# Optimization experiments

Measured on AMD Instinct MI355X. Metric: run time of the kernel, lower is better.

The kernel has to match this reference:

```python
import jax, jax.numpy as jnp
import numpy as np

B, S, D, E = 8, 2048, 1024, 8
TOKENS = B * S
CAPACITY = TOKENS // E  # capacity_factor=1.0, top-1 gating (deepspeed default)


def _moe_layer(x_flat, Wg, We, be):
    """DeepSpeed-style top-1 MoE: gate -> capacity drop -> dispatch -> expert GEMM -> combine.
    x_flat: [T, D]; Wg: [D, E]; We: [E, D, D]; be: [E, D]."""
    gates = jax.nn.softmax(x_flat @ Wg, axis=-1)              # [T, E]
    idx = jnp.argmax(gates, axis=1)                            # [T] expert per token
    mask = jax.nn.one_hot(idx, E, dtype=jnp.int32)             # [T, E]
    loc = jnp.cumsum(mask, axis=0) - 1                         # position within expert
    loc_s = jnp.sum(loc * mask, axis=1)                        # [T]
    keep = loc_s < CAPACITY                                    # capacity drop
    gate_s = jnp.sum(gates * mask.astype(gates.dtype), axis=1) * keep.astype(gates.dtype)
    slot = jnp.clip(loc_s, 0, CAPACITY - 1)
    # dispatch: scatter kept tokens into [E, C, D] buffer (slots are unique for kept tokens)
    disp = jnp.zeros((E, CAPACITY, D), x_flat.dtype).at[idx, slot].add(
        x_flat * keep[:, None].astype(x_flat.dtype))
    # grouped expert GEMM
    eo = jnp.einsum('ecd,edf->ecf', disp, We) + be[:, None, :]  # [E, C, D]
    # combine: gather each token's expert output, scale by its gate value
    return eo[idx, slot] * gate_s[:, None]                      # [T, D]


def reference(x, y, W1, b1, Wg2, We2, be2, Wg3, We3, be3):
    h = jnp.einsum('bsd,df->bsf', x, W1) + b1                  # dense pre-layer
    hf = h.reshape(TOKENS, D)
    o = _moe_layer(hf, Wg2, We2, be2)
    o = _moe_layer(o, Wg3, We3, be3)
    h = h + o.reshape(B, S, D)                                 # residual add
    sent = h.mean(axis=1)                                      # [B, D]
    logp = jax.nn.log_softmax(sent, axis=-1)
    return -jnp.mean(logp[jnp.arange(B), y])                   # CrossEntropyLoss


def setup_inputs() -> dict:
    key = jax.random.key(0)
    ks = jax.random.split(key, 10)
    s = 0.02
    return {
        'x': jax.random.normal(ks[0], (B, S, D), jnp.float32),
        'y': jax.random.randint(ks[1], (B,), 0, D),
        'W1': jax.random.normal(ks[2], (D, D), jnp.float32) * s,
        'b1': jnp.zeros((D,), jnp.float32),
        'Wg2': jax.random.normal(ks[3], (D, E), jnp.float32) * s,
        'We2': jax.random.normal(ks[4], (E, D, D), jnp.float32) * s,
        'be2': jnp.zeros((E, D), jnp.float32),
        'Wg3': jax.random.normal(ks[5], (D, E), jnp.float32) * s,
        'We3': jax.random.normal(ks[6], (E, D, D), jnp.float32) * s,
        'be3': jnp.zeros((E, D), jnp.float32),
    }
```

## Files before the change

kernel.cpp:

```cpp
#include <hip/hip_runtime.h>
#include <hip/hip_bf16.h>
#include <math.h>


#define TOKS 16384
#define DIM 1024
#define NEXP 8
#define CAP 2048
#define BATCH 8
#define SEQ 2048

typedef __bf16 bf16_t;
typedef __bf16 bf16x8 __attribute__((ext_vector_type(8)));
typedef float fx4 __attribute__((ext_vector_type(4)));

__device__ __forceinline__ void gll16(const bf16_t* g, bf16_t* l) {
  __builtin_amdgcn_global_load_lds(
      (const __attribute__((address_space(1))) unsigned int*)g,
      (__attribute__((address_space(3))) unsigned int*)l, 16, 0, 0);
}

#define PW_BLOCKS (17 * 256)
#define CVT_BLOCKS (TOKS * DIM / 8 / 256)
#define PREP_GRID (PW_BLOCKS + 2 + CVT_BLOCKS + 1)
__global__ __launch_bounds__(256) void k_prep(
    const float* __restrict__ W1, const float* __restrict__ We2,
    const float* __restrict__ We3, const float* __restrict__ Wg2,
    const float* __restrict__ Wg3, const float* __restrict__ x,
    bf16_t* __restrict__ Wt, bf16_t* __restrict__ WgP,
    bf16_t* __restrict__ xb, uint4* __restrict__ zreg, int znq) {
  const int id = blockIdx.x;
  const int tid = threadIdx.x;
  if (id < PW_BLOCKS) {
    __shared__ float t[64][65];
    const int m = id >> 8, rem = id & 255;
    const int n0 = (rem & 15) * 64, k0 = (rem >> 4) * 64;
    const float* src = (m == 0) ? W1
                       : (m <= 8) ? We2 + (size_t)(m - 1) * DIM * DIM
                                  : We3 + (size_t)(m - 9) * DIM * DIM;
    bf16_t* dst = Wt + (size_t)m * DIM * DIM;
    const int r = tid >> 4, c4 = (tid & 15) * 4;
#pragma unroll
    for (int i = 0; i < 4; i++) {
      float4 v = *(const float4*)&src[(size_t)(k0 + i * 16 + r) * DIM + n0 + c4];
      t[i * 16 + r][c4] = v.x;
      t[i * 16 + r][c4 + 1] = v.y;
      t[i * 16 + r][c4 + 2] = v.z;
      t[i * 16 + r][c4 + 3] = v.w;
    }
    __syncthreads();
#pragma unroll
    for (int i = 0; i < 4; i++) {
      int rn = i * 16 + r;
      union { bf16_t b[4]; uint2 u; } tmp;
#pragma unroll
      for (int j = 0; j < 4; j++) tmp.b[j] = (bf16_t)t[c4 + j][rn];
      *(uint2*)&dst[(size_t)(n0 + rn) * DIM + k0 + c4] = tmp.u;
    }
  } else if (id < PW_BLOCKS + 2) {
    const int which = id - PW_BLOCKS;
    const float* src = which ? Wg3 : Wg2;
    bf16_t* dst = WgP + which * (128 * 8 * 8);
#pragma unroll
    for (int j = 0; j < 4; j++) {
      int d = tid * 4 + j;
      float4 a = *(const float4*)&src[d * 8];
      float4 b = *(const float4*)&src[d * 8 + 4];
      float v[8] = {a.x, a.y, a.z, a.w, b.x, b.y, b.z, b.w};
#pragma unroll
      for (int e = 0; e < 8; e++)
        dst[((d >> 3) * 8 + e) * 8 + (d & 7)] = (bf16_t)v[e];
    }
  } else if (id < PW_BLOCKS + 2 + CVT_BLOCKS) {
    const int cid = id - PW_BLOCKS - 2;
    size_t i = ((size_t)cid * 256 + tid) * 8;
    float4 a = *(const float4*)&x[i];
    float4 b = *(const float4*)&x[i + 4];
    union { bf16_t h[8]; uint4 u; } t;
    t.h[0] = (bf16_t)a.x; t.h[1] = (bf16_t)a.y; t.h[2] = (bf16_t)a.z; t.h[3] = (bf16_t)a.w;
    t.h[4] = (bf16_t)b.x; t.h[5] = (bf16_t)b.y; t.h[6] = (bf16_t)b.z; t.h[7] = (bf16_t)b.w;
    *(uint4*)&xb[i] = t.u;
  } else {
    const uint4 z = {0u, 0u, 0u, 0u};
    for (int i = tid; i < znq; i += 256) zreg[i] = z;
  }
}

__global__ __launch_bounds__(256) void k_gemm_dense(
    const bf16_t* __restrict__ A, const bf16_t* __restrict__ Bt,
    const float* __restrict__ bias, bf16_t* __restrict__ out,
    float* __restrict__ sent) {
  __shared__ alignas(16) bf16_t As[128 * 64];
  __shared__ alignas(16) bf16_t Bs[128 * 64];
  const int tid = threadIdx.x;
  const int lane = tid & 63, wave = tid >> 6;
  const int quad = lane >> 4, l15 = lane & 15;
  const int wr = (wave >> 1) * 64, wc = (wave & 1) * 64;
  const int id = blockIdx.x;
  const int j_ = id >> 3;
  const int m0 = ((id & 7) * 16 + (j_ >> 3)) * 128;
  const int n0 = (j_ & 7) * 128;
  const int kc = (tid & 7) ^ ((tid >> 3) & 7);
  const int rbase = tid >> 3;

  const bf16_t* gA[4]; const bf16_t* gB[4]; bf16_t* lA[4]; bf16_t* lB[4];
#pragma unroll
  for (int i = 0; i < 4; i++) {
    int r = rbase + 32 * i;
    gA[i] = A + (size_t)(m0 + r) * DIM + kc * 8;
    gB[i] = Bt + (size_t)(n0 + r) * DIM + kc * 8;
    lA[i] = &As[(wave * 64 + 256 * i) * 8];
    lB[i] = &Bs[(wave * 64 + 256 * i) * 8];
  }
  fx4 acc[4][4];
#pragma unroll
  for (int i = 0; i < 4; i++)
#pragma unroll
    for (int j = 0; j < 4; j++) acc[i][j] = (fx4)0.0f;

  for (int k0 = 0; k0 < DIM; k0 += 64) {
#pragma unroll
    for (int i = 0; i < 4; i++) gll16(gA[i] + k0, lA[i]);
#pragma unroll
    for (int i = 0; i < 4; i++) gll16(gB[i] + k0, lB[i]);
    __syncthreads();
#pragma unroll
    for (int s = 0; s < 2; s++) {
      const int pofs = ((s * 4 + quad) ^ (l15 & 7)) << 3;
      bf16x8 av[4], bv[4];
#pragma unroll
      for (int i = 0; i < 4; i++)
        av[i] = *(const bf16x8*)&As[(wr + i * 16 + l15) * 64 + pofs];
#pragma unroll
      for (int j = 0; j < 4; j++)
        bv[j] = *(const bf16x8*)&Bs[(wc + j * 16 + l15) * 64 + pofs];
#pragma unroll
      for (int i = 0; i < 4; i++)
#pragma unroll
        for (int j = 0; j < 4; j++)
          acc[i][j] = __builtin_amdgcn_mfma_f32_16x16x32_bf16(av[i], bv[j], acc[i][j], 0, 0, 0);
    }
    __syncthreads();
  }
  float bb[4], sj[4] = {0.f, 0.f, 0.f, 0.f};
#pragma unroll
  for (int j = 0; j < 4; j++) bb[j] = bias[n0 + wc + j * 16 + l15];
#pragma unroll
  for (int i = 0; i < 4; i++)
#pragma unroll
    for (int r = 0; r < 4; r++) {
      int rowL = wr + i * 16 + quad * 4 + r;
#pragma unroll
      for (int j = 0; j < 4; j++) {
        float v = acc[i][j][r] + bb[j];
        sj[j] += v;
        out[(size_t)(m0 + rowL) * DIM + n0 + wc + j * 16 + l15] = (bf16_t)v;
      }
    }
#pragma unroll
  for (int j = 0; j < 4; j++) {
    sj[j] += __shfl_xor(sj[j], 16);
    sj[j] += __shfl_xor(sj[j], 32);
  }
  if (quad == 0) {
#pragma unroll
    for (int j = 0; j < 4; j++)
      atomicAdd(&sent[(m0 >> 11) * DIM + n0 + wc + j * 16 + l15],
                sj[j] * (1.0f / SEQ));
  }
}

__global__ __launch_bounds__(256) void k_gate_mm(
    const bf16_t* __restrict__ act, const bf16_t* __restrict__ WgPx,
    int* __restrict__ idx, float* __restrict__ gate) {
  __shared__ alignas(16) bf16_t As[64 * 64];
  __shared__ alignas(16) bf16_t WgS[128 * 64];
  __shared__ float L[64][8];
  const int tid = threadIdx.x;
  const int lane = tid & 63, wave = tid >> 6;
  const int quad = lane >> 4, l15 = lane & 15;
  const int m0 = blockIdx.x * 64;
  const int kc = (tid & 7) ^ ((tid >> 3) & 7);
  const int rbase = tid >> 3;

#pragma unroll
  for (int j = 0; j < 4; j++)
    gll16(WgPx + (j * 256 + wave * 64 + lane) * 8, &WgS[(j * 256 + wave * 64) * 8]);

  const bf16_t* gA[2]; bf16_t* lA[2];
#pragma unroll
  for (int i = 0; i < 2; i++) {
    gA[i] = act + (size_t)(m0 + rbase + 32 * i) * DIM + kc * 8;
    lA[i] = &As[wave * 512 + i * 2048];
  }
  fx4 acc = (fx4)0.0f;
  for (int k0 = 0; k0 < DIM; k0 += 64) {
#pragma unroll
    for (int i = 0; i < 2; i++) gll16(gA[i] + k0, lA[i]);
    __syncthreads();
#pragma unroll
    for (int s = 0; s < 2; s++) {
      const int pofs = ((s * 4 + quad) ^ (l15 & 7)) << 3;
      bf16x8 av = *(const bf16x8*)&As[(wave * 16 + l15) * 64 + pofs];
      bf16x8 bv = *(const bf16x8*)&WgS[((k0 >> 3) + s * 4 + quad) * 64 + (l15 & 7) * 8];
      acc = __builtin_amdgcn_mfma_f32_16x16x32_bf16(av, bv, acc, 0, 0, 0);
    }
    __syncthreads();
  }
  if (l15 < 8) {
#pragma unroll
    for (int r = 0; r < 4; r++) L[wave * 16 + quad * 4 + r][l15] = acc[r];
  }
  __syncthreads();
  if (tid < 64) {
    float lg[8];
#pragma unroll
    for (int e = 0; e < 8; e++) lg[e] = L[tid][e];
    float best = lg[0];
    int bi = 0;
#pragma unroll
    for (int e = 1; e < 8; e++)
      if (lg[e] > best) { best = lg[e]; bi = e; }
    float s = 0.f;
#pragma unroll
    for (int e = 0; e < 8; e++) s += expf(lg[e] - best);
    idx[m0 + tid] = bi;
    gate[m0 + tid] = 1.0f / s;
  }
}

#define DLMAX 2048
__global__ __launch_bounds__(1024) void k_route(
    const int* __restrict__ idx, int* __restrict__ tok, int* __restrict__ cnt,
    bf16_t* __restrict__ obuf) {
  const int e = blockIdx.x;
  const int tid = threadIdx.x, lane = tid & 63, wv = tid >> 6;
  __shared__ int wsum[16];
  __shared__ int dlist[DLMAX];
  const int4* p = (const int4*)(idx + tid * 16);
  int m[16];
  int c = 0;
#pragma unroll
  for (int j = 0; j < 4; j++) {
    int4 v = p[j];
    m[j * 4 + 0] = (v.x == e);
    m[j * 4 + 1] = (v.y == e);
    m[j * 4 + 2] = (v.z == e);
    m[j * 4 + 3] = (v.w == e);
    c += m[j * 4] + m[j * 4 + 1] + m[j * 4 + 2] + m[j * 4 + 3];
  }
  int sc = c;
#pragma unroll
  for (int off = 1; off < 64; off <<= 1) {
    int n = __shfl_up(sc, off);
    if (lane >= off) sc += n;
  }
  if (lane == 63) wsum[wv] = sc;
  __syncthreads();
  int wb = 0, tot = 0;
#pragma unroll
  for (int i = 0; i < 16; i++) {
    int s = wsum[i];
    tot += s;
    if (i < wv) wb += s;
  }
  int pos = wb + sc - c;
  const uint4 z = {0u, 0u, 0u, 0u};
#pragma unroll
  for (int j = 0; j < 16; j++) {
    if (m[j]) {
      int t = tid * 16 + j;
      if (pos < CAP) {
        tok[e * CAP + pos] = t;
      } else {
        int di = pos - CAP;
        if (di < DLMAX) dlist[di] = t;
        else
          for (int k = 0; k < 128; k++) *(uint4*)&obuf[(size_t)t * DIM + k * 8] = z;
      }
      pos++;
    }
  }
  if (tid == 0) cnt[e] = tot < CAP ? tot : CAP;
  __syncthreads();
  int ndl = tot - CAP;
  ndl = ndl < 0 ? 0 : (ndl > DLMAX ? DLMAX : ndl);
  for (int d = tid >> 7; d < ndl; d += 8) {
    int t = dlist[d];
    *(uint4*)&obuf[(size_t)t * DIM + (tid & 127) * 8] = z;
  }
}

__global__ __launch_bounds__(256) void k_gemm_expert(
    const bf16_t* __restrict__ Ain, const bf16_t* __restrict__ Wt8,
    const float* __restrict__ be, const int* __restrict__ tok,
    const int* __restrict__ cnt, const float* __restrict__ gate,
    const bf16_t* __restrict__ zp, bf16_t* __restrict__ outp) {
  const int id = blockIdx.x;
  const int e = id & 7;
  const int j_ = id >> 3;
  const int c0 = (j_ >> 3) * 128;
  const int n0 = (j_ & 7) * 128;
  const int count = cnt[e];
  if (c0 >= count) return;
  const bf16_t* Bt = Wt8 + (size_t)e * DIM * DIM;
  const float* bias = be + (size_t)e * DIM;
  const int* tk = tok + e * CAP;

  __shared__ alignas(16) bf16_t As[128 * 64];
  __shared__ alignas(16) bf16_t Bs[128 * 64];
  const int tid = threadIdx.x;
  const int lane = tid & 63, wave = tid >> 6;
  const int quad = lane >> 4, l15 = lane & 15;
  const int wr = (wave >> 1) * 64, wc = (wave & 1) * 64;
  const int kc = (tid & 7) ^ ((tid >> 3) & 7);
  const int rbase = tid >> 3;

  const bf16_t* gA[4]; const bf16_t* gB[4]; bf16_t* lA[4]; bf16_t* lB[4];
#pragma unroll
  for (int i = 0; i < 4; i++) {
    int r = rbase + 32 * i;
    int ca = c0 + r;
    gA[i] = (ca < count) ? Ain + (size_t)tk[ca] * DIM + kc * 8 : zp;
    gB[i] = Bt + (size_t)(n0 + r) * DIM + kc * 8;
    lA[i] = &As[(wave * 64 + 256 * i) * 8];
    lB[i] = &Bs[(wave * 64 + 256 * i) * 8];
  }
  fx4 acc[4][4];
#pragma unroll
  for (int i = 0; i < 4; i++)
#pragma unroll
    for (int j = 0; j < 4; j++) acc[i][j] = (fx4)0.0f;

  for (int k0 = 0; k0 < DIM; k0 += 64) {
#pragma unroll
    for (int i = 0; i < 4; i++) gll16(gA[i] + k0, lA[i]);
#pragma unroll
    for (int i = 0; i < 4; i++) gll16(gB[i] + k0, lB[i]);
    __syncthreads();
#pragma unroll
    for (int s = 0; s < 2; s++) {
      const int pofs = ((s * 4 + quad) ^ (l15 & 7)) << 3;
      bf16x8 av[4], bv[4];
#pragma unroll
      for (int i = 0; i < 4; i++)
        av[i] = *(const bf16x8*)&As[(wr + i * 16 + l15) * 64 + pofs];
#pragma unroll
      for (int j = 0; j < 4; j++)
        bv[j] = *(const bf16x8*)&Bs[(wc + j * 16 + l15) * 64 + pofs];
#pragma unroll
      for (int i = 0; i < 4; i++)
#pragma unroll
        for (int j = 0; j < 4; j++)
          acc[i][j] = __builtin_amdgcn_mfma_f32_16x16x32_bf16(av[i], bv[j], acc[i][j], 0, 0, 0);
    }
    __syncthreads();
  }
  float bb[4];
#pragma unroll
  for (int j = 0; j < 4; j++) bb[j] = bias[n0 + wc + j * 16 + l15];
#pragma unroll
  for (int i = 0; i < 4; i++)
#pragma unroll
    for (int r = 0; r < 4; r++) {
      int c = c0 + wr + i * 16 + quad * 4 + r;
      if (c < count) {
        int t = tk[c];
        float g = gate[t];
#pragma unroll
        for (int j = 0; j < 4; j++)
          outp[(size_t)t * DIM + n0 + wc + j * 16 + l15] =
              (bf16_t)((acc[i][j][r] + bb[j]) * g);
      }
    }
}

__global__ __launch_bounds__(256) void k_reduce_loss(
    const bf16_t* __restrict__ o2, float* __restrict__ sent,
    const int* __restrict__ y, int* __restrict__ done,
    float* __restrict__ out) {
  const int tid = threadIdx.x;
  {
    const int job = blockIdx.x;
    const int d8 = (tid & 127) * 8;
    const int sg = tid >> 7;
    const int b = job >> 5;
    const int s0 = (job & 31) * 64 + sg * 32;
    float acc[8] = {0.f, 0.f, 0.f, 0.f, 0.f, 0.f, 0.f, 0.f};
    const size_t base = ((size_t)b * SEQ + s0) * DIM + d8;
    for (int i = 0; i < 32; i++) {
      union { bf16_t v[8]; uint4 u; } oo;
      oo.u = *(const uint4*)&o2[base + (size_t)i * DIM];
#pragma unroll
      for (int j = 0; j < 8; j++) acc[j] += (float)oo.v[j];
    }
#pragma unroll
    for (int j = 0; j < 8; j++)
      atomicAdd(&sent[b * DIM + d8 + j], acc[j] * (1.0f / SEQ));
  }
  __shared__ int isLast;
  __syncthreads();
  if (tid == 0) {
    __threadfence();
    isLast = (atomicAdd(done, 1) == (int)gridDim.x - 1);
  }
  __syncthreads();
  if (!isLast) return;
  __threadfence();
  __shared__ float red[256];
  float total = 0.f;
  for (int b = 0; b < BATCH; b++) {
    const float* sb = sent + b * DIM;
    float m = -1e30f;
    for (int d = tid; d < DIM; d += 256) m = fmaxf(m, sb[d]);
    red[tid] = m;
    __syncthreads();
    for (int s = 128; s; s >>= 1) {
      if (tid < s) red[tid] = fmaxf(red[tid], red[tid + s]);
      __syncthreads();
    }
    m = red[0];
    __syncthreads();
    float sum = 0.f;
    for (int d = tid; d < DIM; d += 256) sum += expf(sb[d] - m);
    red[tid] = sum;
    __syncthreads();
    for (int s = 128; s; s >>= 1) {
      if (tid < s) red[tid] += red[tid + s];
      __syncthreads();
    }
    if (tid == 0) total += m + logf(red[0]) - sb[y[b]];
    __syncthreads();
  }
  if (tid == 0) out[0] = total * (1.0f / BATCH);
}

extern "C" void kernel_launch(void* const* d_in, const int* in_sizes, int n_in,
                              void* d_out, int out_size, void* d_ws, size_t ws_size,
                              hipStream_t stream) {
  (void)in_sizes; (void)n_in; (void)out_size; (void)ws_size;
  const float* x   = (const float*)d_in[0];
  const int*   y   = (const int*)d_in[1];
  const float* W1  = (const float*)d_in[2];
  const float* b1  = (const float*)d_in[3];
  const float* Wg2 = (const float*)d_in[4];
  const float* We2 = (const float*)d_in[5];
  const float* be2 = (const float*)d_in[6];
  const float* Wg3 = (const float*)d_in[7];
  const float* We3 = (const float*)d_in[8];
  const float* be3 = (const float*)d_in[9];

  char* p = (char*)d_ws;
  size_t off = 0;
  auto carve = [&](size_t bytes) -> char* {
    char* r = p + off;
    off += (bytes + 255) & ~(size_t)255;
    return r;
  };
  bf16_t* Wt   = (bf16_t*)carve((size_t)17 * DIM * DIM * 2);
  bf16_t* WgP  = (bf16_t*)carve(2 * 128 * 8 * 8 * 2);
  bf16_t* h    = (bf16_t*)carve((size_t)TOKS * DIM * 2);
  bf16_t* o1   = (bf16_t*)carve((size_t)TOKS * DIM * 2);
  bf16_t* o2   = (bf16_t*)carve((size_t)TOKS * DIM * 2);
  int*    idx  = (int*)carve(TOKS * 4);
  float*  gate = (float*)carve(TOKS * 4);
  int*    tok  = (int*)carve(NEXP * CAP * 4);
  int*    cnt  = (int*)carve(NEXP * 4);
  size_t zoff0 = off;
  float*  sent = (float*)carve(BATCH * DIM * 4);
  bf16_t* zp   = (bf16_t*)carve(4096);
  int*    done = (int*)carve(256);
  size_t zbytes = off - zoff0;
  bf16_t* xb   = o2;

  k_prep<<<PREP_GRID, 256, 0, stream>>>(
      W1, We2, We3, Wg2, Wg3, x, Wt, WgP, xb,
      (uint4*)sent, (int)(zbytes / 16));

  k_gemm_dense<<<(TOKS / 128) * (DIM / 128), 256, 0, stream>>>(
      xb, Wt, b1, h, sent);

  k_gate_mm<<<TOKS / 64, 256, 0, stream>>>(h, WgP, idx, gate);
  k_route<<<NEXP, 1024, 0, stream>>>(idx, tok, cnt, o1);
  k_gemm_expert<<<NEXP * (CAP / 128) * (DIM / 128), 256, 0, stream>>>(
      h, Wt + (size_t)1 * DIM * DIM, be2, tok, cnt, gate, zp, o1);

  k_gate_mm<<<TOKS / 64, 256, 0, stream>>>(o1, WgP + 128 * 8 * 8, idx, gate);
  k_route<<<NEXP, 1024, 0, stream>>>(idx, tok, cnt, o2);
  k_gemm_expert<<<NEXP * (CAP / 128) * (DIM / 128), 256, 0, stream>>>(
      o1, Wt + (size_t)9 * DIM * DIM, be3, tok, cnt, gate, zp, o2);

  k_reduce_loss<<<256, 256, 0, stream>>>(o2, sent, y, done, (float*)d_out);
}
```

Baseline: 394.6 us.

## Replace dense and expert GEMMs with pipelined 256x256 double-buffered tile kernel

```diff
diff --git a/kernel.cpp b/kernel.cpp
--- a/kernel.cpp
+++ b/kernel.cpp
@@ -19,6 +19,10 @@
       (const __attribute__((address_space(1))) unsigned int*)g,
       (__attribute__((address_space(3))) unsigned int*)l, 16, 0, 0);
 }
+
+#define BARRIER() asm volatile("s_barrier" ::: "memory")
+#define LGKM0()   asm volatile("s_waitcnt lgkmcnt(0)" ::: "memory")
+#define VMC(N)    asm volatile("s_waitcnt vmcnt(" #N ")" ::: "memory")
 
 #define PW_BLOCKS (17 * 256)
 #define CVT_BLOCKS (TOKS * DIM / 8 / 256)
@@ -86,87 +90,201 @@
   }
 }
 
-__global__ __launch_bounds__(256) void k_gemm_dense(
-    const bf16_t* __restrict__ A, const bf16_t* __restrict__ Bt,
-    const float* __restrict__ bias, bf16_t* __restrict__ out,
-    float* __restrict__ sent) {
-  __shared__ alignas(16) bf16_t As[128 * 64];
-  __shared__ alignas(16) bf16_t Bs[128 * 64];
+template <int MODE>
+__global__ __launch_bounds__(512) void k_gemm256(
+    const bf16_t* __restrict__ A, const bf16_t* __restrict__ Bt0,
+    const float* __restrict__ bias0, bf16_t* __restrict__ out,
+    float* __restrict__ sent, const int* __restrict__ tok,
+    const int* __restrict__ cnt, const float* __restrict__ gate,
+    const bf16_t* __restrict__ zp) {
+  __shared__ alignas(16) bf16_t As[2][256 * 64];
+  __shared__ alignas(16) bf16_t Bs[2][256 * 64];
   const int tid = threadIdx.x;
   const int lane = tid & 63, wave = tid >> 6;
   const int quad = lane >> 4, l15 = lane & 15;
-  const int wr = (wave >> 1) * 64, wc = (wave & 1) * 64;
+  const int wm = wave >> 2, wn = wave & 3;
   const int id = blockIdx.x;
-  const int j_ = id >> 3;
-  const int m0 = ((id & 7) * 16 + (j_ >> 3)) * 128;
-  const int n0 = (j_ & 7) * 128;
+  const int xcd = id & 7, rem = id >> 3;
+  const int n0 = (rem & 3) * 256;
+
+  int m0;
+  int count = 0;
+  const bf16_t* Bt;
+  const float* bias;
+  const int* tk = nullptr;
+  if constexpr (MODE == 0) {
+    m0 = (xcd * 8 + (rem >> 2)) * 256;
+    Bt = Bt0;
+    bias = bias0;
+  } else {
+    m0 = (rem >> 2) * 256;
+    count = cnt[xcd];
+    if (m0 >= count) return;
+    Bt = Bt0 + (size_t)xcd * DIM * DIM;
+    bias = bias0 + xcd * DIM;
+    tk = tok + xcd * CAP;
+  }
+
   const int kc = (tid & 7) ^ ((tid >> 3) & 7);
   const int rbase = tid >> 3;
 
-  const bf16_t* gA[4]; const bf16_t* gB[4]; bf16_t* lA[4]; bf16_t* lB[4];
-#pragma unroll
-  for (int i = 0; i < 4; i++) {
-    int r = rbase + 32 * i;
-    gA[i] = A + (size_t)(m0 + r) * DIM + kc * 8;
-    gB[i] = Bt + (size_t)(n0 + r) * DIM + kc * 8;
-    lA[i] = &As[(wave * 64 + 256 * i) * 8];
-    lB[i] = &Bs[(wave * 64 + 256 * i) * 8];
-  }
-  fx4 acc[4][4];
-#pragma unroll
-  for (int i = 0; i < 4; i++)
+  const bf16_t* gA[4];
+  const bf16_t* gB[4];
+#pragma unroll
+  for (int h = 0; h < 2; h++)
+#pragma unroll
+    for (int i = 0; i < 2; i++) {
+      const int r = h * 128 + i * 64 + rbase;
+      if constexpr (MODE == 0) {
+        gA[h * 2 + i] = A + (size_t)(m0 + r) * DIM + kc * 8;
+      } else {
+        const int ca = m0 + r;
+        gA[h * 2 + i] = (ca < count) ? A + (size_t)tk[ca] * DIM + kc * 8 : zp;
+      }
+      gB[h * 2 + i] = Bt + (size_t)(n0 + r) * DIM + kc * 8;
+    }
+
+  auto stA = [&](int t, int half) {
+#pragma unroll
+    for (int i = 0; i < 2; i++)
+      gll16(gA[half * 2 + i] + t * 64,
+            &As[t & 1][(half * 128 + i * 64 + wave * 8) * 64]);
+  };
+  auto stB = [&](int t, int half) {
+#pragma unroll
+    for (int i = 0; i < 2; i++)
+      gll16(gB[half * 2 + i] + t * 64,
+            &Bs[t & 1][(half * 128 + i * 64 + wave * 8) * 64]);
+  };
+  auto rdA = [&](bf16x8 (&av)[4][2], int buf, int mh) {
+#pragma unroll
+    for (int mf = 0; mf < 4; mf++)
+#pragma unroll
+      for (int s = 0; s < 2; s++)
+        av[mf][s] = *(const bf16x8*)&As[buf][(wm * 128 + (mh * 4 + mf) * 16 + l15) * 64 +
+                                            (((s * 4 + quad) ^ (l15 & 7)) << 3)];
+  };
+  auto rdB = [&](bf16x8 (&bv)[2][2], int buf, int nh) {
+#pragma unroll
+    for (int nf = 0; nf < 2; nf++)
+#pragma unroll
+      for (int s = 0; s < 2; s++)
+        bv[nf][s] = *(const bf16x8*)&Bs[buf][(wn * 64 + (nh * 2 + nf) * 16 + l15) * 64 +
+                                            (((s * 4 + quad) ^ (l15 & 7)) << 3)];
+  };
+
+  fx4 acc[8][4];
+#pragma unroll
+  for (int i = 0; i < 8; i++)
 #pragma unroll
     for (int j = 0; j < 4; j++) acc[i][j] = (fx4)0.0f;
 
-  for (int k0 = 0; k0 < DIM; k0 += 64) {
-#pragma unroll
-    for (int i = 0; i < 4; i++) gll16(gA[i] + k0, lA[i]);
-#pragma unroll
-    for (int i = 0; i < 4; i++) gll16(gB[i] + k0, lB[i]);
-    __syncthreads();
-#pragma unroll
-    for (int s = 0; s < 2; s++) {
-      const int pofs = ((s * 4 + quad) ^ (l15 & 7)) << 3;
-      bf16x8 av[4], bv[4];
-#pragma unroll
-      for (int i = 0; i < 4; i++)
-        av[i] = *(const bf16x8*)&As[(wr + i * 16 + l15) * 64 + pofs];
-#pragma unroll
-      for (int j = 0; j < 4; j++)
-        bv[j] = *(const bf16x8*)&Bs[(wc + j * 16 + l15) * 64 + pofs];
-#pragma unroll
-      for (int i = 0; i < 4; i++)
-#pragma unroll
-        for (int j = 0; j < 4; j++)
-          acc[i][j] = __builtin_amdgcn_mfma_f32_16x16x32_bf16(av[i], bv[j], acc[i][j], 0, 0, 0);
-    }
-    __syncthreads();
-  }
-  float bb[4], sj[4] = {0.f, 0.f, 0.f, 0.f};
-#pragma unroll
-  for (int j = 0; j < 4; j++) bb[j] = bias[n0 + wc + j * 16 + l15];
-#pragma unroll
-  for (int i = 0; i < 4; i++)
-#pragma unroll
-    for (int r = 0; r < 4; r++) {
-      int rowL = wr + i * 16 + quad * 4 + r;
-#pragma unroll
-      for (int j = 0; j < 4; j++) {
-        float v = acc[i][j][r] + bb[j];
-        sj[j] += v;
-        out[(size_t)(m0 + rowL) * DIM + n0 + wc + j * 16 + l15] = (bf16_t)v;
+  auto mma = [&](bf16x8 (&av)[4][2], bf16x8 (&bv)[2][2], int mh, int nh) {
+    __builtin_amdgcn_s_setprio(1);
+#pragma unroll
+    for (int s = 0; s < 2; s++)
+#pragma unroll
+      for (int mf = 0; mf < 4; mf++)
+#pragma unroll
+        for (int nf = 0; nf < 2; nf++)
+          acc[mh * 4 + mf][nh * 2 + nf] = __builtin_amdgcn_mfma_f32_16x16x32_bf16(
+              av[mf][s], bv[nf][s], acc[mh * 4 + mf][nh * 2 + nf], 0, 0, 0);
+    __builtin_amdgcn_s_setprio(0);
+  };
+
+  stA(0, 0); stA(0, 1); stB(0, 0); stB(0, 1);
+  stB(1, 0); stB(1, 1); stA(1, 0);
+  VMC(6);
+  BARRIER();
+
+  bf16x8 av0[4][2], av1[4][2], bv0[2][2], bv1[2][2];
+#pragma unroll 2
+  for (int t = 0; t < 14; t++) {
+    const int buf = t & 1;
+    rdA(av0, buf, 0); rdB(bv0, buf, 0); rdB(bv1, buf, 1);
+    stA(t + 1, 1);
+    BARRIER(); LGKM0();
+    mma(av0, bv0, 0, 0);
+    BARRIER();
+    stB(t + 2, 0);
+    BARRIER();
+    mma(av0, bv1, 0, 1);
+    BARRIER();
+    rdA(av1, buf, 1);
+    stB(t + 2, 1);
+    BARRIER(); LGKM0();
+    mma(av1, bv1, 1, 1);
+    BARRIER();
+    stA(t + 2, 0);
+    mma(av1, bv0, 1, 0);
+    VMC(6);
+    BARRIER();
+  }
+  {
+    rdA(av0, 0, 0); rdB(bv0, 0, 0); rdB(bv1, 0, 1);
+    stA(15, 1);
+    BARRIER(); LGKM0();
+    mma(av0, bv0, 0, 0);
+    BARRIER();
+    mma(av0, bv1, 0, 1);
+    BARRIER();
+    rdA(av1, 0, 1);
+    BARRIER(); LGKM0();
+    mma(av1, bv1, 1, 1);
+    BARRIER();
+    mma(av1, bv0, 1, 0);
+    VMC(0);
+    BARRIER();
+  }
+  {
+    rdA(av0, 1, 0); rdB(bv0, 1, 0); rdB(bv1, 1, 1); rdA(av1, 1, 1);
+    LGKM0();
+    mma(av0, bv0, 0, 0); mma(av0, bv1, 0, 1);
+    mma(av1, bv1, 1, 1); mma(av1, bv0, 1, 0);
+  }
+
+  float bb[4];
+#pragma unroll
+  for (int nf = 0; nf < 4; nf++) bb[nf] = bias[n0 + wn * 64 + nf * 16 + l15];
+  if constexpr (MODE == 0) {
+    float sj[4] = {0.f, 0.f, 0.f, 0.f};
+#pragma unroll
+    for (int mf = 0; mf < 8; mf++)
+#pragma unroll
+      for (int r = 0; r < 4; r++) {
+        const int rowL = wm * 128 + mf * 16 + quad * 4 + r;
+#pragma unroll
+        for (int nf = 0; nf < 4; nf++) {
+          const float v = acc[mf][nf][r] + bb[nf];
+          sj[nf] += v;
+          out[(size_t)(m0 + rowL) * DIM + n0 + wn * 64 + nf * 16 + l15] = (bf16_t)v;
+        }
       }
-    }
-#pragma unroll
-  for (int j = 0; j < 4; j++) {
-    sj[j] += __shfl_xor(sj[j], 16);
-    sj[j] += __shfl_xor(sj[j], 32);
-  }
-  if (quad == 0) {
-#pragma unroll
-    for (int j = 0; j < 4; j++)
-      atomicAdd(&sent[(m0 >> 11) * DIM + n0 + wc + j * 16 + l15],
-                sj[j] * (1.0f / SEQ));
+#pragma unroll
+    for (int nf = 0; nf < 4; nf++) {
+      sj[nf] += __shfl_xor(sj[nf], 16);
+      sj[nf] += __shfl_xor(sj[nf], 32);
+    }
+    if (quad == 0)
+#pragma unroll
+      for (int nf = 0; nf < 4; nf++)
+        atomicAdd(&sent[(m0 >> 11) * DIM + n0 + wn * 64 + nf * 16 + l15],
+                  sj[nf] * (1.0f / SEQ));
+  } else {
+#pragma unroll
+    for (int mf = 0; mf < 8; mf++)
+#pragma unroll
+      for (int r = 0; r < 4; r++) {
+        const int c = m0 + wm * 128 + mf * 16 + quad * 4 + r;
+        if (c < count) {
+          const int tkn = tk[c];
+          const float g = gate[tkn];
+#pragma unroll
+          for (int nf = 0; nf < 4; nf++)
+            out[(size_t)tkn * DIM + n0 + wn * 64 + nf * 16 + l15] =
+                (bf16_t)((acc[mf][nf][r] + bb[nf]) * g);
+        }
+      }
   }
 }
 
@@ -289,90 +407,6 @@
     int t = dlist[d];
     *(uint4*)&obuf[(size_t)t * DIM + (tid & 127) * 8] = z;
   }
-}
-
-__global__ __launch_bounds__(256) void k_gemm_expert(
-    const bf16_t* __restrict__ Ain, const bf16_t* __restrict__ Wt8,
-    const float* __restrict__ be, const int* __restrict__ tok,
-    const int* __restrict__ cnt, const float* __restrict__ gate,
-    const bf16_t* __restrict__ zp, bf16_t* __restrict__ outp) {
-  const int id = blockIdx.x;
-  const int e = id & 7;
-  const int j_ = id >> 3;
-  const int c0 = (j_ >> 3) * 128;
-  const int n0 = (j_ & 7) * 128;
-  const int count = cnt[e];
-  if (c0 >= count) return;
-  const bf16_t* Bt = Wt8 + (size_t)e * DIM * DIM;
-  const float* bias = be + (size_t)e * DIM;
-  const int* tk = tok + e * CAP;
-
-  __shared__ alignas(16) bf16_t As[128 * 64];
-  __shared__ alignas(16) bf16_t Bs[128 * 64];
-  const int tid = threadIdx.x;
-  const int lane = tid & 63, wave = tid >> 6;
-  const int quad = lane >> 4, l15 = lane & 15;
-  const int wr = (wave >> 1) * 64, wc = (wave & 1) * 64;
-  const int kc = (tid & 7) ^ ((tid >> 3) & 7);
-  const int rbase = tid >> 3;
-
-  const bf16_t* gA[4]; const bf16_t* gB[4]; bf16_t* lA[4]; bf16_t* lB[4];
-#pragma unroll
-  for (int i = 0; i < 4; i++) {
-    int r = rbase + 32 * i;
-    int ca = c0 + r;
-    gA[i] = (ca < count) ? Ain + (size_t)tk[ca] * DIM + kc * 8 : zp;
-    gB[i] = Bt + (size_t)(n0 + r) * DIM + kc * 8;
-    lA[i] = &As[(wave * 64 + 256 * i) * 8];
-    lB[i] = &Bs[(wave * 64 + 256 * i) * 8];
-  }
-  fx4 acc[4][4];
-#pragma unroll
-  for (int i = 0; i < 4; i++)
-#pragma unroll
-    for (int j = 0; j < 4; j++) acc[i][j] = (fx4)0.0f;
-
-  for (int k0 = 0; k0 < DIM; k0 += 64) {
-#pragma unroll
-    for (int i = 0; i < 4; i++) gll16(gA[i] + k0, lA[i]);
-#pragma unroll
-    for (int i = 0; i < 4; i++) gll16(gB[i] + k0, lB[i]);
-    __syncthreads();
-#pragma unroll
-    for (int s = 0; s < 2; s++) {
-      const int pofs = ((s * 4 + quad) ^ (l15 & 7)) << 3;
-      bf16x8 av[4], bv[4];
-#pragma unroll
-      for (int i = 0; i < 4; i++)
-        av[i] = *(const bf16x8*)&As[(wr + i * 16 + l15) * 64 + pofs];
-#pragma unroll
-      for (int j = 0; j < 4; j++)
-        bv[j] = *(const bf16x8*)&Bs[(wc + j * 16 + l15) * 64 + pofs];
-#pragma unroll
-      for (int i = 0; i < 4; i++)
-#pragma unroll
-        for (int j = 0; j < 4; j++)
-          acc[i][j] = __builtin_amdgcn_mfma_f32_16x16x32_bf16(av[i], bv[j], acc[i][j], 0, 0, 0);
-    }
-    __syncthreads();
-  }
-  float bb[4];
-#pragma unroll
-  for (int j = 0; j < 4; j++) bb[j] = bias[n0 + wc + j * 16 + l15];
-#pragma unroll
-  for (int i = 0; i < 4; i++)
-#pragma unroll
-    for (int r = 0; r < 4; r++) {
-      int c = c0 + wr + i * 16 + quad * 4 + r;
-      if (c < count) {
-        int t = tk[c];
-        float g = gate[t];
-#pragma unroll
-        for (int j = 0; j < 4; j++)
-          outp[(size_t)t * DIM + n0 + wc + j * 16 + l15] =
-              (bf16_t)((acc[i][j][r] + bb[j]) * g);
-      }
-    }
 }
 
 __global__ __launch_bounds__(256) void k_reduce_loss(
@@ -477,18 +511,18 @@
       W1, We2, We3, Wg2, Wg3, x, Wt, WgP, xb,
       (uint4*)sent, (int)(zbytes / 16));
 
-  k_gemm_dense<<<(TOKS / 128) * (DIM / 128), 256, 0, stream>>>(
-      xb, Wt, b1, h, sent);
+  k_gemm256<0><<<256, 512, 0, stream>>>(
+      xb, Wt, b1, h, sent, nullptr, nullptr, nullptr, zp);
 
   k_gate_mm<<<TOKS / 64, 256, 0, stream>>>(h, WgP, idx, gate);
   k_route<<<NEXP, 1024, 0, stream>>>(idx, tok, cnt, o1);
-  k_gemm_expert<<<NEXP * (CAP / 128) * (DIM / 128), 256, 0, stream>>>(
-      h, Wt + (size_t)1 * DIM * DIM, be2, tok, cnt, gate, zp, o1);
+  k_gemm256<1><<<256, 512, 0, stream>>>(
+      h, Wt + (size_t)1 * DIM * DIM, be2, o1, nullptr, tok, cnt, gate, zp);
 
   k_gate_mm<<<TOKS / 64, 256, 0, stream>>>(o1, WgP + 128 * 8 * 8, idx, gate);
   k_route<<<NEXP, 1024, 0, stream>>>(idx, tok, cnt, o2);
-  k_gemm_expert<<<NEXP * (CAP / 128) * (DIM / 128), 256, 0, stream>>>(
-      o1, Wt + (size_t)9 * DIM * DIM, be3, tok, cnt, gate, zp, o2);
+  k_gemm256<1><<<256, 512, 0, stream>>>(
+      o1, Wt + (size_t)9 * DIM * DIM, be3, o2, nullptr, tok, cnt, gate, zp);
 
   k_reduce_loss<<<256, 256, 0, stream>>>(o2, sent, y, done, (float*)d_out);
 }
```

After: 378.9 us. 4.0% less time.
